# Kernel tuning notes

Hardware: AMD Instinct MI355X
Metric: run time of the kernel (lower is better)

## Reference

```python
import jax, jax.numpy as jnp
import numpy as np

GRID = 256
SENSORS = 128
TSTEPS = 1024
ROWS = SENSORS * TSTEPS      # 131072
COLS = GRID * GRID           # 65536
NNZ = 30_000_000
GAIN = 1.0


def setup_inputs() -> dict:
    key = jax.random.key(0)
    k1, k2, k3, k4 = jax.random.split(key, 4)
    field_map = jax.random.normal(k1, (GRID, GRID), dtype=jnp.float32)
    idx_row = jax.random.randint(k2, (NNZ,), 0, ROWS, dtype=jnp.int64)
    idx_col = jax.random.randint(k3, (NNZ,), 0, COLS, dtype=jnp.int64)
    vals = jax.random.normal(k4, (NNZ,), dtype=jnp.float32)
    return {"field_map": field_map, "idx_row": idx_row, "idx_col": idx_col, "vals": vals}


def reference(field_map, idx_row, idx_col, vals):
    # column-major flatten: permute(1,0).reshape(-1) in the torch source
    flat_field = field_map.T.reshape(-1)                      # [COLS]
    # fused gather-multiply-scatter: sensor_response = A @ flat_field
    contrib = vals * jnp.take(flat_field, idx_col)            # [NNZ]
    response = jax.ops.segment_sum(contrib, idx_row, num_segments=ROWS)  # [ROWS]
    return (response * GAIN).reshape(TSTEPS, SENSORS)
```

## Files before the change

### kernel.cpp

```cpp
#include <hip/hip_runtime.h>
#include <hip/hip_fp16.h>

#define ROWS_TOTAL 131072
#define NNZ        30000000
#define NGROUPS    (NNZ / 4)

#define NRANGES  8
#define BINS     (ROWS_TOTAL / NRANGES)
#define ATHREADS 1024
#define MAXNB2   64

#define RCAP        3815536
#define GCNT_STRIDE 16

#define PB_THREADS   512
#define PB_BLOCKS    1024
#define CHUNK_GROUPS 1024
#define CHUNK_WORDS  (CHUNK_GROUPS * 4)
#define NCHUNKS      ((NGROUPS + CHUNK_GROUPS - 1) / CHUNK_GROUPS)
#define FCAP         768

__device__ __forceinline__ int colmap(int c) {
    return ((c & 255) << 8) | (c >> 8);
}

__device__ __forceinline__ unsigned pack_pair(int row, float val) {
    unsigned hb = __half_as_ushort(__float2half(val));
    unsigned f15 = (hb + 1u) >> 1;
    return ((unsigned)row << 15) | f15;
}

__device__ __forceinline__ float unpack_val(unsigned w) {
    return __half2float(__ushort_as_half((unsigned short)((w & 0x7FFFu) << 1)));
}

__global__ __launch_bounds__(PB_THREADS) void pack_bin(
    const float* __restrict__ field,
    const int*   __restrict__ idx_row,
    const int*   __restrict__ idx_col,
    const float* __restrict__ vals,
    unsigned*    __restrict__ binned,
    unsigned*    __restrict__ gcnt)
{
    __shared__ __align__(16) unsigned chunk[CHUNK_WORDS];
    __shared__ __align__(16) unsigned fifo[NRANGES][FCAP];

    const int tid  = threadIdx.x;
    const int lane = tid & 63;
    const unsigned wid = (unsigned)(tid >> 6);
    unsigned* const dst = binned + (size_t)wid * RCAP;
    const unsigned long long below = (1ull << lane) - 1ull;

    for (int ck = blockIdx.x; ck < NCHUNKS; ck += gridDim.x) {
        const int gbase = ck * CHUNK_GROUPS;

        #pragma unroll
        for (int h = 0; h < 2; ++h) {
            const int gl = (h << 9) + tid;
            const int gg = gbase + gl;
            uint4 o = make_uint4(0u, 0u, 0u, 0u);
            if (gg < NGROUPS) {
                const int4   r = ((const int4*)idx_row)[gg];
                const int4   c = ((const int4*)idx_col)[gg];
                const float4 v = ((const float4*)vals)[gg];
                o.x = pack_pair(r.x, v.x * field[colmap(c.x)]);
                o.y = pack_pair(r.y, v.y * field[colmap(c.y)]);
                o.z = pack_pair(r.z, v.z * field[colmap(c.z)]);
                o.w = pack_pair(r.w, v.w * field[colmap(c.w)]);
            }
            *(uint4*)&chunk[gl << 2] = o;
        }
        __syncthreads();

        unsigned cnt = 0;
        const uint4* chunk4 = (const uint4*)chunk;
        #pragma unroll 4
        for (int s = 0; s < CHUNK_WORDS / 256; ++s) {
            const uint4 q = chunk4[(s << 6) + lane];
            #define SCAN1(W) {                                                  \
                const unsigned w_ = (W);                                        \
                const bool hit_ = ((w_ >> 29) == wid);                          \
                const unsigned long long m_ = __ballot(hit_);                   \
                if (hit_) {                                                     \
                    const unsigned off_ = cnt + (unsigned)__popcll(m_ & below); \
                    if (off_ < (unsigned)FCAP) fifo[wid][off_] = w_;            \
                    else {  \
                        unsigned gs_ = atomicAdd(&gcnt[wid * GCNT_STRIDE], 4u); \
                        if (gs_ + 4u <= (unsigned)RCAP) {                       \
                            uint4 sp_ = make_uint4(w_, 0u, 0u, 0u);             \
                            *(uint4*)(dst + gs_) = sp_;                         \
                        }                                                       \
                    }                                                           \
                }                                                               \
                cnt += (unsigned)__popcll(m_);                                  \
            }
            SCAN1(q.x); SCAN1(q.y); SCAN1(q.z); SCAN1(q.w);
            #undef SCAN1
        }
        if (cnt > (unsigned)FCAP) cnt = (unsigned)FCAP;
        const unsigned cntR = (cnt + 3u) & ~3u;
        if (lane < (int)(cntR - cnt)) fifo[wid][cnt + (unsigned)lane] = 0u;

        asm volatile("s_waitcnt lgkmcnt(0)" ::: "memory");

        unsigned gs0 = 0;
        if (lane == 0) gs0 = atomicAdd(&gcnt[wid * GCNT_STRIDE], cntR);
        gs0 = __shfl(gs0, 0);

        const unsigned n4 = cntR >> 2;
        const uint4* f4 = (const uint4*)fifo[wid];
        for (unsigned t = (unsigned)lane; t < n4; t += 64u) {
            const unsigned o4 = gs0 + (t << 2);
            if (o4 + 4u <= (unsigned)RCAP)
                *(uint4*)(dst + o4) = f4[t];
        }
        __syncthreads();
    }
}

__global__ __launch_bounds__(ATHREADS) void bin_accum(
    const unsigned* __restrict__ binned,
    const unsigned* __restrict__ gcnt,
    float*          __restrict__ copies,
    int nb2)
{
    __shared__ float bins[BINS];
    const int j = blockIdx.x >> 3;
    const int p = blockIdx.x & 7;

    for (int t = threadIdx.x; t < BINS; t += ATHREADS) bins[t] = 0.0f;
    __syncthreads();

    unsigned n = gcnt[p * GCNT_STRIDE];
    if (n > (unsigned)RCAP) n = (unsigned)RCAP;
    const unsigned n4 = n >> 2;
    const uint4* src = (const uint4*)(binned + (size_t)p * RCAP);
    const int start = (int)(((long long)j       * (long long)n4) / nb2);
    const int end   = (int)(((long long)(j + 1) * (long long)n4) / nb2);
    const unsigned lo = (unsigned)p << 14;

    #pragma unroll 2
    for (int g = start + threadIdx.x; g < end; g += ATHREADS) {
        const uint4 w = src[g];
        unsigned l0 = (w.x >> 15) - lo;
        if (l0 < (unsigned)BINS) atomicAdd(&bins[l0], unpack_val(w.x));
        unsigned l1 = (w.y >> 15) - lo;
        if (l1 < (unsigned)BINS) atomicAdd(&bins[l1], unpack_val(w.y));
        unsigned l2 = (w.z >> 15) - lo;
        if (l2 < (unsigned)BINS) atomicAdd(&bins[l2], unpack_val(w.z));
        unsigned l3 = (w.w >> 15) - lo;
        if (l3 < (unsigned)BINS) atomicAdd(&bins[l3], unpack_val(w.w));
    }
    __syncthreads();

    float* dstc = copies + ((size_t)p * nb2 + j) * BINS;
    for (int t = threadIdx.x; t < BINS; t += ATHREADS) dstc[t] = bins[t];
}

__global__ __launch_bounds__(256) void reduce_copies(
    const float* __restrict__ copies,
    float*       __restrict__ out,
    int nb2)
{
    const int r   = blockIdx.x * 256 + threadIdx.x;
    const int p   = r >> 14;
    const int bin = r & (BINS - 1);
    const float* base = copies + ((size_t)p * nb2) * BINS + bin;
    float s = 0.0f;
    #pragma unroll 16
    for (int j = 0; j < nb2; ++j)
        s += base[(size_t)j * BINS];
    out[r] = s;
}

__global__ void zero_cnt(unsigned* __restrict__ g) {
    g[threadIdx.x] = 0u;
}

__global__ __launch_bounds__(1024) void pack_pairs(
    const float* __restrict__ field,
    const int*   __restrict__ idx_row,
    const int*   __restrict__ idx_col,
    const float* __restrict__ vals,
    unsigned*    __restrict__ pairs)
{
    const int stride = gridDim.x * blockDim.x;
    #pragma unroll 2
    for (int i = blockIdx.x * 1024 + threadIdx.x; i < NGROUPS; i += stride) {
        const int4   r = ((const int4*)idx_row)[i];
        const int4   c = ((const int4*)idx_col)[i];
        const float4 v = ((const float4*)vals)[i];
        uint4 o;
        o.x = pack_pair(r.x, v.x * field[colmap(c.x)]);
        o.y = pack_pair(r.y, v.y * field[colmap(c.y)]);
        o.z = pack_pair(r.z, v.z * field[colmap(c.z)]);
        o.w = pack_pair(r.w, v.w * field[colmap(c.w)]);
        ((uint4*)pairs)[i] = o;
    }
}

__global__ __launch_bounds__(ATHREADS) void range_accum(
    const unsigned* __restrict__ pairs,
    float*          __restrict__ copies,
    int nb2)
{
    __shared__ float bins[BINS];
    const int j  = blockIdx.x >> 3;
    const int p  = blockIdx.x & 7;
    const unsigned lo = (unsigned)p << 14;

    for (int t = threadIdx.x; t < BINS; t += ATHREADS) bins[t] = 0.0f;
    __syncthreads();

    const int start = (int)(((long long)j       * NGROUPS) / nb2);
    const int end   = (int)(((long long)(j + 1) * NGROUPS) / nb2);

    #pragma unroll 2
    for (int g = start + threadIdx.x; g < end; g += ATHREADS) {
        const uint4 w = ((const uint4*)pairs)[g];
        unsigned l0 = (w.x >> 15) - lo;
        if (l0 < (unsigned)BINS) atomicAdd(&bins[l0], unpack_val(w.x));
        unsigned l1 = (w.y >> 15) - lo;
        if (l1 < (unsigned)BINS) atomicAdd(&bins[l1], unpack_val(w.y));
        unsigned l2 = (w.z >> 15) - lo;
        if (l2 < (unsigned)BINS) atomicAdd(&bins[l2], unpack_val(w.z));
        unsigned l3 = (w.w >> 15) - lo;
        if (l3 < (unsigned)BINS) atomicAdd(&bins[l3], unpack_val(w.w));
    }
    __syncthreads();

    float* dst = copies + ((size_t)p * nb2 + j) * BINS;
    for (int t = threadIdx.x; t < BINS; t += ATHREADS) dst[t] = bins[t];
}

__global__ __launch_bounds__(256) void coo_scatter_kernel(
    const float* __restrict__ field,
    const int*   __restrict__ idx_row,
    const int*   __restrict__ idx_col,
    const float* __restrict__ vals,
    float*       __restrict__ out)
{
    const int i = blockIdx.x * 256 + threadIdx.x;
    if (i >= NGROUPS) return;
    const int4   r = ((const int4*)idx_row)[i];
    const int4   c = ((const int4*)idx_col)[i];
    const float4 v = ((const float4*)vals)[i];
    atomicAdd(&out[r.x], v.x * field[colmap(c.x)]);
    atomicAdd(&out[r.y], v.y * field[colmap(c.y)]);
    atomicAdd(&out[r.z], v.z * field[colmap(c.z)]);
    atomicAdd(&out[r.w], v.w * field[colmap(c.w)]);
}

extern "C" void kernel_launch(void* const* d_in, const int* in_sizes, int n_in,
                              void* d_out, int out_size, void* d_ws, size_t ws_size,
                              hipStream_t stream) {
    const float* field   = (const float*)d_in[0];
    const int*   idx_row = (const int*)d_in[1];
    const int*   idx_col = (const int*)d_in[2];
    const float* vals    = (const float*)d_in[3];
    float*       out     = (float*)d_out;

    const size_t binned_bytes = (size_t)NRANGES * RCAP * sizeof(unsigned);
    const size_t cnt_bytes    = 1024;
    const size_t pair_bytes   = (size_t)NNZ * sizeof(unsigned);
    const size_t copy_slice   = (size_t)NRANGES * BINS * sizeof(float);

    if (ws_size >= binned_bytes + cnt_bytes + 2 * copy_slice) {
        unsigned* binned = (unsigned*)d_ws;
        unsigned* gcnt   = (unsigned*)((char*)d_ws + binned_bytes);
        float*    copies = (float*)((char*)d_ws + binned_bytes + cnt_bytes);

        int nb2 = (int)((ws_size - binned_bytes - cnt_bytes) / copy_slice);
        if (nb2 > MAXNB2) nb2 = MAXNB2;

        zero_cnt<<<1, NRANGES * GCNT_STRIDE, 0, stream>>>(gcnt);
        pack_bin<<<PB_BLOCKS, PB_THREADS, 0, stream>>>(field, idx_row, idx_col,
                                                       vals, binned, gcnt);
        bin_accum<<<nb2 * NRANGES, ATHREADS, 0, stream>>>(binned, gcnt, copies, nb2);
        reduce_copies<<<ROWS_TOTAL / 256, 256, 0, stream>>>(copies, out, nb2);
    } else if (ws_size >= pair_bytes + 2 * copy_slice) {
        unsigned* pairs  = (unsigned*)d_ws;
        float*    copies = (float*)((char*)d_ws + pair_bytes);

        int nb2 = (int)((ws_size - pair_bytes) / copy_slice);
        if (nb2 > MAXNB2) nb2 = MAXNB2;

        pack_pairs<<<512, 1024, 0, stream>>>(field, idx_row, idx_col, vals, pairs);
        range_accum<<<nb2 * NRANGES, ATHREADS, 0, stream>>>(pairs, copies, nb2);
        reduce_copies<<<ROWS_TOTAL / 256, 256, 0, stream>>>(copies, out, nb2);
    } else {
        hipMemsetAsync(out, 0, (size_t)out_size * sizeof(float), stream);
        coo_scatter_kernel<<<(NGROUPS + 255) / 256, 256, 0, stream>>>(
            field, idx_row, idx_col, vals, out);
    }
}
```

Before: 619.3 us.

## Software-pipeline chunk loads and gathers in pack_bin; unroll bin_accum deeper

New measurement: 583.6 us. -5.8%, faster.

```diff
diff --git a/kernel.cpp b/kernel.cpp
--- a/kernel.cpp
+++ b/kernel.cpp
@@ -51,26 +51,53 @@
     unsigned* const dst = binned + (size_t)wid * RCAP;
     const unsigned long long below = (1ull << lane) - 1ull;
 
-    for (int ck = blockIdx.x; ck < NCHUNKS; ck += gridDim.x) {
-        const int gbase = ck * CHUNK_GROUPS;
-
-        #pragma unroll
-        for (int h = 0; h < 2; ++h) {
-            const int gl = (h << 9) + tid;
-            const int gg = gbase + gl;
-            uint4 o = make_uint4(0u, 0u, 0u, 0u);
-            if (gg < NGROUPS) {
-                const int4   r = ((const int4*)idx_row)[gg];
-                const int4   c = ((const int4*)idx_col)[gg];
-                const float4 v = ((const float4*)vals)[gg];
-                o.x = pack_pair(r.x, v.x * field[colmap(c.x)]);
-                o.y = pack_pair(r.y, v.y * field[colmap(c.y)]);
-                o.z = pack_pair(r.z, v.z * field[colmap(c.z)]);
-                o.w = pack_pair(r.w, v.w * field[colmap(c.w)]);
-            }
-            *(uint4*)&chunk[gl << 2] = o;
-        }
+    const int c0 = (int)(((long long)blockIdx.x       * NCHUNKS) / gridDim.x);
+    const int c1 = (int)(((long long)(blockIdx.x + 1) * NCHUNKS) / gridDim.x);
+
+    #define LDGRP(G, R, C, V) {                                              \
+        if ((G) < NGROUPS) {                                                 \
+            R = ((const int4*)idx_row)[(G)];                                 \
+            C = ((const int4*)idx_col)[(G)];                                 \
+            V = ((const float4*)vals)[(G)];                                  \
+        } else {                                                             \
+            const int b_ = (G) << 2;                                         \
+            R.x = ( b_      << 5) & 131071; R.y = ((b_ + 1) << 5) & 131071;  \
+            R.z = ((b_ + 2) << 5) & 131071; R.w = ((b_ + 3) << 5) & 131071;  \
+            C = make_int4(0, 0, 0, 0);                                       \
+            V = make_float4(0.f, 0.f, 0.f, 0.f);                             \
+        } }
+
+    #define LOADREG(CK) {                                                    \
+        const int gA_ = (CK) * CHUNK_GROUPS + tid;                           \
+        const int gB_ = gA_ + PB_THREADS;                                    \
+        LDGRP(gA_, ra, ca, va);                                              \
+        LDGRP(gB_, rb, cb, vb); }
+
+    #define GATHERS() {                                                      \
+        fa0 = va.x * field[colmap(ca.x)]; fa1 = va.y * field[colmap(ca.y)];  \
+        fa2 = va.z * field[colmap(ca.z)]; fa3 = va.w * field[colmap(ca.w)];  \
+        fb0 = vb.x * field[colmap(cb.x)]; fb1 = vb.y * field[colmap(cb.y)];  \
+        fb2 = vb.z * field[colmap(cb.z)]; fb3 = vb.w * field[colmap(cb.w)]; }
+
+    int4 ra, ca, rb, cb;
+    float4 va, vb;
+    float fa0, fa1, fa2, fa3, fb0, fb1, fb2, fb3;
+
+    LOADREG(c0);
+    GATHERS();
+
+    for (int ck = c0; ck < c1; ++ck) {
+        uint4 oA, oB;
+        oA.x = pack_pair(ra.x, fa0); oA.y = pack_pair(ra.y, fa1);
+        oA.z = pack_pair(ra.z, fa2); oA.w = pack_pair(ra.w, fa3);
+        oB.x = pack_pair(rb.x, fb0); oB.y = pack_pair(rb.y, fb1);
+        oB.z = pack_pair(rb.z, fb2); oB.w = pack_pair(rb.w, fb3);
+        *(uint4*)&chunk[(unsigned)tid << 2]                  = oA;
+        *(uint4*)&chunk[(unsigned)(PB_THREADS + tid) << 2]   = oB;
         __syncthreads();
+
+        const bool more = (ck + 1 < c1);
+        if (more) LOADREG(ck + 1);
 
         unsigned cnt = 0;
         const uint4* chunk4 = (const uint4*)chunk;
@@ -101,6 +128,8 @@
         const unsigned cntR = (cnt + 3u) & ~3u;
         if (lane < (int)(cntR - cnt)) fifo[wid][cnt + (unsigned)lane] = 0u;
 
+        if (more) GATHERS();
+
         asm volatile("s_waitcnt lgkmcnt(0)" ::: "memory");
 
         unsigned gs0 = 0;
@@ -116,6 +145,9 @@
         }
         __syncthreads();
     }
+    #undef LOADREG
+    #undef LDGRP
+    #undef GATHERS
 }
 
 __global__ __launch_bounds__(ATHREADS) void bin_accum(
@@ -139,7 +171,7 @@
     const int end   = (int)(((long long)(j + 1) * (long long)n4) / nb2);
     const unsigned lo = (unsigned)p << 14;
 
-    #pragma unroll 2
+    #pragma unroll 4
     for (int g = start + threadIdx.x; g < end; g += ATHREADS) {
         const uint4 w = src[g];
         unsigned l0 = (w.x >> 15) - lo;
```
